# Optimization experiments

Hardware: AMD Instinct MI355X
Metric: run time of the kernel (lower is better)

The kernel has to match this reference:

```python
import jax, jax.numpy as jnp
import numpy as np

N_EXPERTS = 8
DIM = 2048
INTER = 1408
TOTAL_TOKENS = 16384
ALPHA = 1.702
LIMIT = 7.0
LINEAR_OFFSET = 1.0


def setup_inputs() -> dict:
    key = jax.random.key(0)
    k1, k2, k3, k4 = jax.random.split(key, 4)
    x = jax.random.normal(k1, (TOTAL_TOKENS, DIM), dtype=jnp.float32)
    permuted_probs = jax.random.uniform(k2, (TOTAL_TOKENS, 1), dtype=jnp.float32)
    # Stacked-transposed views as in gate_and_up_projs / down_projs properties:
    # [E, in_features, out_features]
    gate_up_w = jax.random.normal(k3, (N_EXPERTS, DIM, 2 * INTER), dtype=jnp.float32) * (DIM ** -0.5)
    down_w = jax.random.normal(k4, (N_EXPERTS, INTER, DIM), dtype=jnp.float32) * (INTER ** -0.5)
    tokens_per_expert = jnp.full((N_EXPERTS,), TOTAL_TOKENS // N_EXPERTS, dtype=jnp.int32)
    return {"x": x, "permuted_probs": permuted_probs, "gate_up_w": gate_up_w,
            "down_w": down_w, "tokens_per_expert": tokens_per_expert}


def quick_geglu(h, probs):
    # interleaved split, as x[..., ::2] / x[..., 1::2]
    gate = jnp.minimum(h[..., ::2], LIMIT)
    up = jnp.clip(h[..., 1::2], -LIMIT, LIMIT)
    glu = gate * jax.nn.sigmoid(ALPHA * gate)
    inter = glu * (up + LINEAR_OFFSET)
    return (inter * probs).astype(h.dtype)


def reference(x, permuted_probs, gate_up_w, down_w, tokens_per_expert):
    # tokens are pre-permuted: equal static group sizes per expert (fp8 pad/unpad
    # is an identity on the math; grouped GEMM expressed as batched einsum).
    E = gate_up_w.shape[0]
    xr = x.reshape(E, -1, DIM)                      # [E, T, dim]
    h = jnp.einsum('etd,edf->etf', xr, gate_up_w)   # [E, T, 2*inter]
    probs = permuted_probs.reshape(E, -1, 1)
    act = quick_geglu(h, probs)                     # [E, T, inter]
    out = jnp.einsum('eti,eio->eto', act, down_w)   # [E, T, dim]
    return out.reshape(-1, DIM)
```

## Files before the change

### kernel.cpp

```cpp
#include <hip/hip_runtime.h>
#include <hip/hip_bf16.h>
#include <stdint.h>

#define N_EXPERTS 8
#define DIM 2048
#define INTER 1408
#define NGU (2*INTER)
#define TOK_E 2048
#define TOTAL_TOKENS 16384

typedef __attribute__((ext_vector_type(8))) short short8;
typedef __attribute__((ext_vector_type(4))) float f32x4;

__device__ __forceinline__ unsigned short f2bf(float f) {
    union { float f; unsigned u; } v; v.f = f;
    unsigned r = v.u + 0x7FFF + ((v.u >> 16) & 1);
    return (unsigned short)(r >> 16);
}

#define GLOAD16(G, L) __builtin_amdgcn_global_load_lds( \
    (const __attribute__((address_space(1))) void*)(G), \
    (__attribute__((address_space(3))) void*)(L), 16, 0, 0)


__global__ void convert_x(const float* __restrict__ in, unsigned short* __restrict__ out, int n8) {
    int i = blockIdx.x * blockDim.x + threadIdx.x;
    int stride = gridDim.x * blockDim.x;
    for (; i < n8; i += stride) {
        const float4* p = (const float4*)(in + (size_t)i * 8);
        float4 v0 = p[0], v1 = p[1];
        union { unsigned short u[8]; uint4 q; } o;
        o.u[0]=f2bf(v0.x); o.u[1]=f2bf(v0.y); o.u[2]=f2bf(v0.z); o.u[3]=f2bf(v0.w);
        o.u[4]=f2bf(v1.x); o.u[5]=f2bf(v1.y); o.u[6]=f2bf(v1.z); o.u[7]=f2bf(v1.w);
        *(uint4*)(out + (size_t)i * 8) = o.q;
    }
}

__global__ __launch_bounds__(256)
void transpose_convert(const float* __restrict__ in, unsigned short* __restrict__ out,
                       int K, int N, int permute) {
    __shared__ float tile[32][129];
    const int n0 = blockIdx.x * 32, k0 = blockIdx.y * 128;
    const size_t ein  = (size_t)blockIdx.z * K * N;
    const size_t eout = (size_t)blockIdx.z * N * K;
    const int tc = threadIdx.x & 31;
    const int tr = threadIdx.x >> 5;
    #pragma unroll
    for (int i = 0; i < 16; ++i) {
        int k = tr + i * 8;
        tile[tc][k] = in[ein + (size_t)(k0 + k) * N + n0 + tc];
    }
    __syncthreads();
    const int kg = threadIdx.x & 31;
    const int r0 = threadIdx.x >> 5;
    #pragma unroll
    for (int i = 0; i < 4; ++i) {
        int r = r0 + i * 8;
        int c = n0 + r;
        int dr = c;
        if (permute) {
            int a = c >> 1;
            dr = ((a >> 4) << 5) + (a & 15) + ((c & 1) << 4);
        }
        union { unsigned short u[4]; uint2 q; } o;
        #pragma unroll
        for (int j = 0; j < 4; ++j) o.u[j] = f2bf(tile[r][kg * 4 + j]);
        *(uint2*)(out + eout + (size_t)dr * K + k0 + kg * 4) = o.q;
    }
}


#define SB0 __builtin_amdgcn_sched_barrier(0)
#define VMC(N_) asm volatile("s_waitcnt vmcnt(" #N_ ")" ::: "memory")
#define LGK8 asm volatile("s_waitcnt lgkmcnt(8)" ::: "memory")

#define GEMM_PROLOG(LDKC) \
    const int t = threadIdx.x; \
    const int lane = t & 63, wid = t >> 6; \
    const int wm = wid >> 2, wn = wid & 3;             \
    const int l15 = lane & 15; \
    const int rd0 = (lane & 15) * 64 + (((lane >> 4) ^ (lane & 7)) * 8); \
    const int rd1 = (lane & 15) * 64 + ((((lane >> 4) + 4) ^ (lane & 7)) * 8); \
    const size_t goff = (size_t)(t >> 3) * (LDKC) + (size_t)(((t & 7) ^ ((t >> 3) & 7)) * 8); \
    const int ldsw = wid * 512 + lane * 8;

#define STGA(LDKC, bb_, h_, kt_) do { \
    const unsigned short* g_ = gA + (size_t)(h_) * 128 * (LDKC) + (size_t)(kt_) * 64 + goff; \
    unsigned short* l_ = sA + (bb_) * 16384 + (h_) * 8192 + ldsw; \
    GLOAD16(g_, l_); GLOAD16(g_ + (size_t)64 * (LDKC), l_ + 4096); \
} while (0)

#define STGB(LDKC, bb_, h_, kt_) do { \
    const unsigned short* g_ = gB + (size_t)(h_) * 128 * (LDKC) + (size_t)(kt_) * 64 + goff; \
    unsigned short* l_ = sB + (bb_) * 16384 + (h_) * 8192 + ldsw; \
    GLOAD16(g_, l_); GLOAD16(g_ + (size_t)64 * (LDKC), l_ + 4096); \
} while (0)

#define DSA2(bb_, qm_) do { \
    const unsigned short* p_ = &sA[(bb_) * 16384 + ((qm_) * 128 + wm * 64) * 64]; \
    _Pragma("unroll") for (int m_ = 0; m_ < 4; ++m_) { \
        a[m_][0] = *(const short8*)(p_ + m_ * 1024 + rd0); \
        a[m_][1] = *(const short8*)(p_ + m_ * 1024 + rd1); } \
} while (0)

#define DSB2(bb_, qn_, R_) do { \
    const unsigned short* p_ = &sB[(bb_) * 16384 + ((qn_) * 128 + wn * 32) * 64]; \
    _Pragma("unroll") for (int n_ = 0; n_ < 2; ++n_) { \
        R_[n_][0] = *(const short8*)(p_ + n_ * 1024 + rd0); \
        R_[n_][1] = *(const short8*)(p_ + n_ * 1024 + rd1); } \
} while (0)

#define QMF(qm_, qn_, B_) do { \
    _Pragma("unroll") for (int k_ = 0; k_ < 2; ++k_) { \
        _Pragma("unroll") for (int m_ = 0; m_ < 4; ++m_) { \
            _Pragma("unroll") for (int n_ = 0; n_ < 2; ++n_) { \
                acc[qm_][qn_][m_][n_] = __builtin_amdgcn_mfma_f32_16x16x32_bf16(a[m_][k_], B_[n_][k_], acc[qm_][qn_][m_][n_], 0, 0, 0); \
            } } } \
} while (0)

#define PH(DSOPS, STGOPS, MFOPS, ENDOPS) do { \
    DSOPS; \
    STGOPS; \
    SB0; \
    asm volatile("s_waitcnt lgkmcnt(0)" ::: "memory"); \
    ENDOPS; \
    SB0; \
    __builtin_amdgcn_s_barrier(); \
    __builtin_amdgcn_s_setprio(1); \
    MFOPS; \
    __builtin_amdgcn_s_setprio(0); \
    SB0; \
} while (0)

#define ITER8(LDKC, kt0_, SG2, SG3, SG4, SG5, SG6, SG7, SG8, E4, E8) \
    PH(DSA2(0,0); DSB2(0,0,bq0); LGK8, STGA(LDKC,1,1,(kt0_)+1), QMF(0,0,bq0), ); \
    PH(DSB2(0,1,bq1),            SG2,                     QMF(0,1,bq1), ); \
    PH(DSA2(0,1),                SG3,                     QMF(1,0,bq0), ); \
    PH(,                         SG4,                     QMF(1,1,bq1), E4); \
    PH(DSA2(1,0); DSB2(1,0,bq0); LGK8, SG5,               QMF(0,0,bq0), ); \
    PH(DSB2(1,1,bq1),            SG6,                     QMF(0,1,bq1), ); \
    PH(DSA2(1,1),                SG7,                     QMF(1,0,bq0), ); \
    PH(,                         SG8,                     QMF(1,1,bq1), E8);

#define GEMM_PIPE(LDKC, NI_) \
    short8 a[4][2], bq0[2][2], bq1[2][2]; \
    f32x4 acc[2][2][4][2]; \
    _Pragma("unroll") for (int q_ = 0; q_ < 2; ++q_) \
    _Pragma("unroll") for (int r_ = 0; r_ < 2; ++r_) \
    _Pragma("unroll") for (int m_ = 0; m_ < 4; ++m_) \
    _Pragma("unroll") for (int n_ = 0; n_ < 2; ++n_) acc[q_][r_][m_][n_] = (f32x4)0.0f; \
     \
    STGA(LDKC,0,0,0); STGB(LDKC,0,0,0); STGB(LDKC,0,1,0); STGA(LDKC,0,1,0); \
    STGA(LDKC,1,0,1); STGB(LDKC,1,0,1); STGB(LDKC,1,1,1); \
    VMC(6); \
    __builtin_amdgcn_s_barrier(); \
    for (int it = 0; it < (NI_) - 1; ++it) { \
        const int kt0 = 2 * it; \
        ITER8(LDKC, kt0, \
              STGA(LDKC,0,0,kt0+2), STGB(LDKC,0,0,kt0+2), STGB(LDKC,0,1,kt0+2), STGA(LDKC,0,1,kt0+2), \
              STGA(LDKC,1,0,kt0+3), STGB(LDKC,1,0,kt0+3), STGB(LDKC,1,1,kt0+3), \
              VMC(6), VMC(6)) \
    } \
    { \
        const int kt0 = 2 * ((NI_) - 1); \
        ITER8(LDKC, kt0, , , , , , , , VMC(0), ) \
    }


__global__ __launch_bounds__(512, 2)
void gemm_gu(const unsigned short* __restrict__ A,
             const unsigned short* __restrict__ Bt,
             const float* __restrict__ probs,
             unsigned short* __restrict__ act) {
    __shared__ unsigned short sA[2 * 16384];
    __shared__ unsigned short sB[2 * 16384];
    GEMM_PROLOG(DIM)
    const int bid = blockIdx.x;
    const int e = bid & 7;
    const int local = bid >> 3;
    const int tm = local & 7;
    const int tn = local >> 3;
    const unsigned short* gA = A  + (size_t)(e * TOK_E + tm * 256) * DIM;
    const unsigned short* gB = Bt + (size_t)e * NGU * DIM + (size_t)(tn * 256) * DIM;

    GEMM_PIPE(DIM, 16)

    const int rgrp = lane >> 4;
    #pragma unroll
    for (int qm = 0; qm < 2; ++qm) {
        #pragma unroll
        for (int qn = 0; qn < 2; ++qn) {
            const int acol = tn * 128 + qn * 64 + wn * 16 + l15;
            #pragma unroll
            for (int m = 0; m < 4; ++m) {
                const int row0 = e * TOK_E + tm * 256 + qm * 128 + wm * 64 + m * 16 + rgrp * 4;
                #pragma unroll
                for (int j = 0; j < 4; ++j) {
                    float p = probs[row0 + j];
                    float g = fminf(acc[qm][qn][m][0][j], 7.0f);
                    float u = fminf(fmaxf(acc[qm][qn][m][1][j], -7.0f), 7.0f);
                    float glu = g / (1.0f + __expf(-1.702f * g));
                    float r = glu * (u + 1.0f) * p;
                    act[(size_t)(row0 + j) * INTER + acol] = f2bf(r);
                }
            }
        }
    }
}


__global__ __launch_bounds__(512, 2)
void gemm_down(const unsigned short* __restrict__ A,
               const unsigned short* __restrict__ Bt,
               float* __restrict__ out) {
    __shared__ unsigned short sA[2 * 16384];
    __shared__ unsigned short sB[2 * 16384];
    GEMM_PROLOG(INTER)
    const int bid = blockIdx.x;
    const int e = bid & 7;
    const int local = bid >> 3;
    const int tm = local & 7;
    const int tn = local >> 3;
    const unsigned short* gA = A  + (size_t)(e * TOK_E + tm * 256) * INTER;
    const unsigned short* gB = Bt + (size_t)e * DIM * INTER + (size_t)(tn * 256) * INTER;

    GEMM_PIPE(INTER, 11)

    const int rgrp = lane >> 4;
    #pragma unroll
    for (int qm = 0; qm < 2; ++qm) {
        #pragma unroll
        for (int qn = 0; qn < 2; ++qn) {
            #pragma unroll
            for (int m = 0; m < 4; ++m) {
                const int row0 = e * TOK_E + tm * 256 + qm * 128 + wm * 64 + m * 16 + rgrp * 4;
                #pragma unroll
                for (int j = 0; j < 4; ++j) {
                    #pragma unroll
                    for (int n = 0; n < 2; ++n) {
                        const int col = tn * 256 + qn * 128 + wn * 32 + n * 16 + l15;
                        out[(size_t)(row0 + j) * DIM + col] = acc[qm][qn][m][n][j];
                    }
                }
            }
        }
    }
}


extern "C" void kernel_launch(void* const* d_in, const int* in_sizes, int n_in,
                              void* d_out, int out_size, void* d_ws, size_t ws_size,
                              hipStream_t stream) {
    const float* x     = (const float*)d_in[0];
    const float* probs = (const float*)d_in[1];
    const float* gup   = (const float*)d_in[2];
    const float* dwn   = (const float*)d_in[3];
    float* out = (float*)d_out;

    char* ws = (char*)d_ws;
    const size_t SZ_XB  = (size_t)TOTAL_TOKENS * DIM * 2;
    const size_t SZ_GUB = (size_t)N_EXPERTS * NGU * DIM * 2;
    const size_t SZ_DWB = (size_t)N_EXPERTS * DIM * INTER * 2;
    unsigned short* xb   = (unsigned short*)(ws);
    unsigned short* gub  = (unsigned short*)(ws + SZ_XB);
    unsigned short* dwb  = (unsigned short*)(ws + SZ_XB + SZ_GUB);
    unsigned short* actb = (unsigned short*)(ws + SZ_XB + SZ_GUB + SZ_DWB);

    convert_x<<<2048, 256, 0, stream>>>(x, xb, TOTAL_TOKENS * DIM / 8);

    dim3 tg1(NGU / 32, DIM / 128, N_EXPERTS);
    transpose_convert<<<tg1, 256, 0, stream>>>(gup, gub, DIM, NGU, 1);
    dim3 tg2(DIM / 32, INTER / 128, N_EXPERTS);
    transpose_convert<<<tg2, 256, 0, stream>>>(dwn, dwb, INTER, DIM, 0);

    gemm_gu<<<704, 512, 0, stream>>>(xb, gub, probs, actb);
    gemm_down<<<512, 512, 0, stream>>>(actb, dwb, out);
}
```

Before: 400.2 us.

## Switch GEMMs to 4-wave blocks with 128x128 per-wave tiles and ping-pong fragments

Both grouped GEMMs now run with 256-thread blocks (4 waves in a 2x2 layout) instead of 8 waves, so each wave owns a 128x128 output sub-tile with 4x4 MFMA fragments. This raises register-level operand reuse and halves the share of LDS reads per MFMA. The schedule is rebuilt as MFMA-first windows that prefetch the next A/B fragments into double-buffered registers while global-to-LDS loads are issued, with one barrier per window. The cost is far more accumulator registers, one block per CU (lower occupancy) and fewer waves to hide latency.

```diff
diff --git a/kernel.cpp b/kernel.cpp
--- a/kernel.cpp
+++ b/kernel.cpp
@@ -72,12 +72,11 @@
 
 #define SB0 __builtin_amdgcn_sched_barrier(0)
 #define VMC(N_) asm volatile("s_waitcnt vmcnt(" #N_ ")" ::: "memory")
-#define LGK8 asm volatile("s_waitcnt lgkmcnt(8)" ::: "memory")
 
 #define GEMM_PROLOG(LDKC) \
     const int t = threadIdx.x; \
     const int lane = t & 63, wid = t >> 6; \
-    const int wm = wid >> 2, wn = wid & 3;             \
+    const int wm = wid >> 1, wn = wid & 1;             \
     const int l15 = lane & 15; \
     const int rd0 = (lane & 15) * 64 + (((lane >> 4) ^ (lane & 7)) * 8); \
     const int rd1 = (lane & 15) * 64 + ((((lane >> 4) + 4) ^ (lane & 7)) * 8); \
@@ -85,89 +84,89 @@
     const int ldsw = wid * 512 + lane * 8;
 
 #define STGA(LDKC, bb_, h_, kt_) do { \
-    const unsigned short* g_ = gA + (size_t)(h_) * 128 * (LDKC) + (size_t)(kt_) * 64 + goff; \
-    unsigned short* l_ = sA + (bb_) * 16384 + (h_) * 8192 + ldsw; \
-    GLOAD16(g_, l_); GLOAD16(g_ + (size_t)64 * (LDKC), l_ + 4096); \
+    const unsigned short* g_ = gA + (size_t)(h_) * 64 * (LDKC) + (size_t)(kt_) * 64 + goff; \
+    unsigned short* l_ = sA + (bb_) * 16384 + (h_) * 4096 + ldsw; \
+    GLOAD16(g_, l_);                               GLOAD16(g_ + (size_t)32 * (LDKC), l_ + 2048); \
+    GLOAD16(g_ + (size_t)128 * (LDKC), l_ + 8192); GLOAD16(g_ + (size_t)160 * (LDKC), l_ + 10240); \
 } while (0)
 
 #define STGB(LDKC, bb_, h_, kt_) do { \
-    const unsigned short* g_ = gB + (size_t)(h_) * 128 * (LDKC) + (size_t)(kt_) * 64 + goff; \
-    unsigned short* l_ = sB + (bb_) * 16384 + (h_) * 8192 + ldsw; \
-    GLOAD16(g_, l_); GLOAD16(g_ + (size_t)64 * (LDKC), l_ + 4096); \
-} while (0)
-
-#define DSA2(bb_, qm_) do { \
-    const unsigned short* p_ = &sA[(bb_) * 16384 + ((qm_) * 128 + wm * 64) * 64]; \
+    const unsigned short* g_ = gB + (size_t)(h_) * 64 * (LDKC) + (size_t)(kt_) * 64 + goff; \
+    unsigned short* l_ = sB + (bb_) * 16384 + (h_) * 4096 + ldsw; \
+    GLOAD16(g_, l_);                               GLOAD16(g_ + (size_t)32 * (LDKC), l_ + 2048); \
+    GLOAD16(g_ + (size_t)128 * (LDKC), l_ + 8192); GLOAD16(g_ + (size_t)160 * (LDKC), l_ + 10240); \
+} while (0)
+
+#define DSA2(bb_, qm_, DST_) do { \
+    const unsigned short* p_ = &sA[(bb_) * 16384 + (wm * 128 + (qm_) * 64) * 64]; \
     _Pragma("unroll") for (int m_ = 0; m_ < 4; ++m_) { \
-        a[m_][0] = *(const short8*)(p_ + m_ * 1024 + rd0); \
-        a[m_][1] = *(const short8*)(p_ + m_ * 1024 + rd1); } \
-} while (0)
-
-#define DSB2(bb_, qn_, R_) do { \
-    const unsigned short* p_ = &sB[(bb_) * 16384 + ((qn_) * 128 + wn * 32) * 64]; \
-    _Pragma("unroll") for (int n_ = 0; n_ < 2; ++n_) { \
-        R_[n_][0] = *(const short8*)(p_ + n_ * 1024 + rd0); \
-        R_[n_][1] = *(const short8*)(p_ + n_ * 1024 + rd1); } \
-} while (0)
-
-#define QMF(qm_, qn_, B_) do { \
+        DST_[m_][0] = *(const short8*)(p_ + m_ * 1024 + rd0); \
+        DST_[m_][1] = *(const short8*)(p_ + m_ * 1024 + rd1); } \
+} while (0)
+
+#define DSB2(bb_, qn_, DST_) do { \
+    const unsigned short* p_ = &sB[(bb_) * 16384 + (wn * 128 + (qn_) * 64) * 64]; \
+    _Pragma("unroll") for (int n_ = 0; n_ < 4; ++n_) { \
+        DST_[n_][0] = *(const short8*)(p_ + n_ * 1024 + rd0); \
+        DST_[n_][1] = *(const short8*)(p_ + n_ * 1024 + rd1); } \
+} while (0)
+
+#define QMF(qm_, qn_, A_, B_) do { \
     _Pragma("unroll") for (int k_ = 0; k_ < 2; ++k_) { \
         _Pragma("unroll") for (int m_ = 0; m_ < 4; ++m_) { \
-            _Pragma("unroll") for (int n_ = 0; n_ < 2; ++n_) { \
-                acc[qm_][qn_][m_][n_] = __builtin_amdgcn_mfma_f32_16x16x32_bf16(a[m_][k_], B_[n_][k_], acc[qm_][qn_][m_][n_], 0, 0, 0); \
+            _Pragma("unroll") for (int n_ = 0; n_ < 4; ++n_) { \
+                acc[qm_][qn_][m_][n_] = __builtin_amdgcn_mfma_f32_16x16x32_bf16(A_[m_][k_], B_[n_][k_], acc[qm_][qn_][m_][n_], 0, 0, 0); \
             } } } \
 } while (0)
 
-#define PH(DSOPS, STGOPS, MFOPS, ENDOPS) do { \
-    DSOPS; \
-    STGOPS; \
-    SB0; \
-    asm volatile("s_waitcnt lgkmcnt(0)" ::: "memory"); \
-    ENDOPS; \
-    SB0; \
-    __builtin_amdgcn_s_barrier(); \
+#define WIN(MF_, DS_, STG_, END_) do { \
     __builtin_amdgcn_s_setprio(1); \
-    MFOPS; \
+    MF_; \
     __builtin_amdgcn_s_setprio(0); \
     SB0; \
-} while (0)
-
-#define ITER8(LDKC, kt0_, SG2, SG3, SG4, SG5, SG6, SG7, SG8, E4, E8) \
-    PH(DSA2(0,0); DSB2(0,0,bq0); LGK8, STGA(LDKC,1,1,(kt0_)+1), QMF(0,0,bq0), ); \
-    PH(DSB2(0,1,bq1),            SG2,                     QMF(0,1,bq1), ); \
-    PH(DSA2(0,1),                SG3,                     QMF(1,0,bq0), ); \
-    PH(,                         SG4,                     QMF(1,1,bq1), E4); \
-    PH(DSA2(1,0); DSB2(1,0,bq0); LGK8, SG5,               QMF(0,0,bq0), ); \
-    PH(DSB2(1,1,bq1),            SG6,                     QMF(0,1,bq1), ); \
-    PH(DSA2(1,1),                SG7,                     QMF(1,0,bq0), ); \
-    PH(,                         SG8,                     QMF(1,1,bq1), E8);
+    DS_; \
+    STG_; \
+    SB0; \
+    END_; \
+    __builtin_amdgcn_s_barrier(); \
+} while (0)
+
+#define ITER(SG1,SG2,SG3,SG4,SG5,SG6,SG7,SG8, E5,E8, DS8) \
+    WIN(QMF(0,0,a0,b0), DSA2(0,1,a1),                SG1, VMC(4)); \
+    WIN(QMF(1,0,a1,b0), DSB2(0,1,b1),                SG2, );       \
+    WIN(QMF(0,1,a0,b1), ,                            SG3, VMC(4)); \
+    WIN(QMF(1,1,a1,b1), DSA2(1,0,a0); DSB2(1,0,b0),  SG4, VMC(4)); \
+    WIN(QMF(0,0,a0,b0), DSA2(1,1,a1),                SG5, E5);     \
+    WIN(QMF(1,0,a1,b0), DSB2(1,1,b1),                SG6, );       \
+    WIN(QMF(0,1,a0,b1), ,                            SG7, E8);     \
+    WIN(QMF(1,1,a1,b1), DS8,                         SG8, E8);
 
 #define GEMM_PIPE(LDKC, NI_) \
-    short8 a[4][2], bq0[2][2], bq1[2][2]; \
-    f32x4 acc[2][2][4][2]; \
+    short8 a0[4][2], a1[4][2], b0[4][2], b1[4][2]; \
+    f32x4 acc[2][2][4][4]; \
     _Pragma("unroll") for (int q_ = 0; q_ < 2; ++q_) \
     _Pragma("unroll") for (int r_ = 0; r_ < 2; ++r_) \
     _Pragma("unroll") for (int m_ = 0; m_ < 4; ++m_) \
-    _Pragma("unroll") for (int n_ = 0; n_ < 2; ++n_) acc[q_][r_][m_][n_] = (f32x4)0.0f; \
+    _Pragma("unroll") for (int n_ = 0; n_ < 4; ++n_) acc[q_][r_][m_][n_] = (f32x4)0.0f; \
      \
-    STGA(LDKC,0,0,0); STGB(LDKC,0,0,0); STGB(LDKC,0,1,0); STGA(LDKC,0,1,0); \
-    STGA(LDKC,1,0,1); STGB(LDKC,1,0,1); STGB(LDKC,1,1,1); \
-    VMC(6); \
+    STGA(LDKC,0,0,0); STGB(LDKC,0,0,0); STGA(LDKC,0,1,0); STGB(LDKC,0,1,0); \
+    VMC(4); \
     __builtin_amdgcn_s_barrier(); \
+    DSA2(0,0,a0); DSB2(0,0,b0); \
     for (int it = 0; it < (NI_) - 1; ++it) { \
         const int kt0 = 2 * it; \
-        ITER8(LDKC, kt0, \
-              STGA(LDKC,0,0,kt0+2), STGB(LDKC,0,0,kt0+2), STGB(LDKC,0,1,kt0+2), STGA(LDKC,0,1,kt0+2), \
-              STGA(LDKC,1,0,kt0+3), STGB(LDKC,1,0,kt0+3), STGB(LDKC,1,1,kt0+3), \
-              VMC(6), VMC(6)) \
+        ITER(STGA(LDKC,1,0,kt0+1), STGB(LDKC,1,0,kt0+1), STGA(LDKC,1,1,kt0+1), STGB(LDKC,1,1,kt0+1), \
+             STGA(LDKC,0,0,kt0+2), STGB(LDKC,0,0,kt0+2), STGA(LDKC,0,1,kt0+2), STGB(LDKC,0,1,kt0+2), \
+             VMC(4), VMC(4), DSA2(0,0,a0); DSB2(0,0,b0)) \
     } \
-    { \
+    {  \
         const int kt0 = 2 * ((NI_) - 1); \
-        ITER8(LDKC, kt0, , , , , , , , VMC(0), ) \
-    }
-
-
-__global__ __launch_bounds__(512, 2)
+        ITER(STGA(LDKC,1,0,kt0+1), STGB(LDKC,1,0,kt0+1), STGA(LDKC,1,1,kt0+1), STGB(LDKC,1,1,kt0+1), \
+             , , , , VMC(0), , ) \
+    }
+
+
+__global__ __launch_bounds__(256, 1)
 void gemm_gu(const unsigned short* __restrict__ A,
              const unsigned short* __restrict__ Bt,
              const float* __restrict__ probs,
@@ -190,18 +189,21 @@
     for (int qm = 0; qm < 2; ++qm) {
         #pragma unroll
         for (int qn = 0; qn < 2; ++qn) {
-            const int acol = tn * 128 + qn * 64 + wn * 16 + l15;
             #pragma unroll
             for (int m = 0; m < 4; ++m) {
-                const int row0 = e * TOK_E + tm * 256 + qm * 128 + wm * 64 + m * 16 + rgrp * 4;
+                const int row0 = e * TOK_E + tm * 256 + wm * 128 + qm * 64 + m * 16 + rgrp * 4;
                 #pragma unroll
                 for (int j = 0; j < 4; ++j) {
                     float p = probs[row0 + j];
-                    float g = fminf(acc[qm][qn][m][0][j], 7.0f);
-                    float u = fminf(fmaxf(acc[qm][qn][m][1][j], -7.0f), 7.0f);
-                    float glu = g / (1.0f + __expf(-1.702f * g));
-                    float r = glu * (u + 1.0f) * p;
-                    act[(size_t)(row0 + j) * INTER + acol] = f2bf(r);
+                    #pragma unroll
+                    for (int pr = 0; pr < 2; ++pr) {
+                        float g = fminf(acc[qm][qn][m][2 * pr][j], 7.0f);
+                        float u = fminf(fmaxf(acc[qm][qn][m][2 * pr + 1][j], -7.0f), 7.0f);
+                        float glu = g / (1.0f + __expf(-1.702f * g));
+                        float rv = glu * (u + 1.0f) * p;
+                        const int acol = tn * 128 + wn * 64 + qn * 32 + pr * 16 + l15;
+                        act[(size_t)(row0 + j) * INTER + acol] = f2bf(rv);
+                    }
                 }
             }
         }
@@ -209,7 +211,7 @@
 }
 
 
-__global__ __launch_bounds__(512, 2)
+__global__ __launch_bounds__(256, 1)
 void gemm_down(const unsigned short* __restrict__ A,
                const unsigned short* __restrict__ Bt,
                float* __restrict__ out) {
@@ -233,12 +235,12 @@
         for (int qn = 0; qn < 2; ++qn) {
             #pragma unroll
             for (int m = 0; m < 4; ++m) {
-                const int row0 = e * TOK_E + tm * 256 + qm * 128 + wm * 64 + m * 16 + rgrp * 4;
+                const int row0 = e * TOK_E + tm * 256 + wm * 128 + qm * 64 + m * 16 + rgrp * 4;
                 #pragma unroll
                 for (int j = 0; j < 4; ++j) {
                     #pragma unroll
-                    for (int n = 0; n < 2; ++n) {
-                        const int col = tn * 256 + qn * 128 + wn * 32 + n * 16 + l15;
+                    for (int n = 0; n < 4; ++n) {
+                        const int col = tn * 256 + wn * 128 + qn * 64 + n * 16 + l15;
                         out[(size_t)(row0 + j) * DIM + col] = acc[qm][qn][m][n][j];
                     }
                 }
@@ -273,6 +275,6 @@
     dim3 tg2(DIM / 32, INTER / 128, N_EXPERTS);
     transpose_convert<<<tg2, 256, 0, stream>>>(dwn, dwb, INTER, DIM, 0);
 
-    gemm_gu<<<704, 512, 0, stream>>>(xb, gub, probs, actb);
-    gemm_down<<<512, 512, 0, stream>>>(actb, dwb, out);
-}
+    gemm_gu<<<704, 256, 0, stream>>>(xb, gub, probs, actb);
+    gemm_down<<<512, 256, 0, stream>>>(actb, dwb, out);
+}
```

Result: slower. 520.4 us (+30.0%).
